# Kernel optimization log

Measured on AMD Instinct MI355X. Metric: run time of the kernel, lower is better.

Reference implementation:

```python
import jax, jax.numpy as jnp
import numpy as np

SCALE_XY = 1.2           # yolo1 in Yolov4Head
OBJ_THRESH = 0.5         # b_o >= 0.5 gate in post_process
BOX_SCORE_THRESH = 0.05
NMS_THRESH = 0.7         # rpn_nms_thresh
MAX_DET = 300            # fixed capacity for jit-compatible NMS


def _decode(x, anchors):
    # x: [B, A*(5+C), H, W] -> boxes [B,H,W,A,4] (xyxy, normalized), obj logits, class logits
    b, c, h, w = x.shape
    a = anchors.shape[0]
    nc = c // a - 5
    out = x.reshape(b, a, 5 + nc, h, w).transpose(0, 3, 4, 1, 2)  # [B,H,W,A,5+C]
    cx = jnp.arange(w, dtype=x.dtype).reshape(1, 1, w, 1)
    cy = jnp.arange(h, dtype=x.dtype).reshape(1, h, 1, 1)
    xy = SCALE_XY * jax.nn.sigmoid(out[..., :2]) - 0.5 * (SCALE_XY - 1)
    bx = (xy[..., 0] + cx) / w
    by = (xy[..., 1] + cy) / h
    b_xy = jnp.stack([bx, by], axis=-1)
    b_wh = jnp.clip(jnp.exp(out[..., 2:4]) * anchors.reshape(1, 1, 1, a, 2), 0.0, 2.0)
    tl = b_xy - 0.5 * b_wh
    boxes = jnp.concatenate([tl, tl + b_wh], axis=-1)  # [B,H,W,A,4]
    return boxes, out[..., 4], out[..., 5:]


def _iou_one_vs_all(box, boxes):
    lt = jnp.maximum(box[:2], boxes[:, :2])
    rb = jnp.minimum(box[2:], boxes[:, 2:])
    wh = jnp.clip(rb - lt, 0.0)
    inter = wh[:, 0] * wh[:, 1]
    a1 = (box[2] - box[0]) * (box[3] - box[1])
    a2 = (boxes[:, 2] - boxes[:, 0]) * (boxes[:, 3] - boxes[:, 1])
    return inter / (a1 + a2 - inter + 1e-9)


def _post_process_single(boxes, b_o, b_scores):
    # boxes [N,4], b_o [N], b_scores [N,C]; fixed-size equivalent of YoloLayer.post_process
    obj = jax.nn.sigmoid(b_o)
    cls = jax.nn.sigmoid(b_scores)
    boxes = jnp.clip(boxes, 0.0, 1.0)
    labels = jnp.argmax(cls, axis=-1)
    score = jnp.max(cls, axis=-1) * obj
    valid = (obj >= OBJ_THRESH) & (score >= BOX_SCORE_THRESH)
    masked = jnp.where(valid, score, -1.0)
    _, top_i = jax.lax.top_k(masked, MAX_DET)
    sel_boxes = boxes[top_i]
    sel_labels = labels[top_i]
    sel_valid = valid[top_i]
    sel_scores = jnp.where(sel_valid, score[top_i], 0.0)
    pos = jnp.arange(MAX_DET)

    def body(i, keep):
        iou = _iou_one_vs_all(sel_boxes[i], sel_boxes)
        suppress = (iou > NMS_THRESH) & keep[i] & (pos > i)
        return keep & (~suppress)

    keep = jax.lax.fori_loop(0, MAX_DET, body, sel_valid)
    return sel_boxes, sel_scores, sel_labels, keep


def setup_inputs() -> dict:
    key = jax.random.key(0)
    k1, _ = jax.random.split(key)
    x = jax.random.normal(k1, (32, 255, 76, 76), dtype=jnp.float32)
    anchors = jnp.array([[12.0, 16.0], [19.0, 36.0], [40.0, 28.0]], dtype=jnp.float32) / 608.0
    return {"x": x, "anchors": anchors}


def reference(x, anchors):
    boxes, b_o, b_s = _decode(x, anchors)
    b = x.shape[0]
    nc = b_s.shape[-1]
    boxes = boxes.reshape(b, -1, 4)
    b_o = b_o.reshape(b, -1)
    b_s = b_s.reshape(b, -1, nc)
    det_boxes, det_scores, det_labels, keep = jax.vmap(_post_process_single)(boxes, b_o, b_s)
    return det_boxes, det_scores, det_labels, keep
```

## Files before the change

### kernel.cpp

```cpp
#include <hip/hip_runtime.h>
#include <stdint.h>

#define BATCH   32
#define GRID_HW 5776
#define NA      3
#define NPB     (NA*GRID_HW)
#define NCLS    80
#define MAXDET  300
#define NBINS   4096
#define CANDN   512
#define T2      1024
#define CHUNK   17
#define NQ      (BATCH*NPB/4)
#define S4      (GRID_HW/4)

__device__ __forceinline__ float sigf(float x){ return 1.0f/(1.0f + expf(-x)); }

__device__ __forceinline__ int binf(float v){
    if (v < 0.0f) return 0;
    int b = (int)(v * 4096.0f);
    return b > (NBINS-1) ? (NBINS-1) : b;
}

__device__ __forceinline__ unsigned int ordf(float v){
    unsigned int u = __float_as_uint(v);
    return (u & 0x80000000u) ? ~u : (u | 0x80000000u);
}

__global__ void zero_hist_kernel(unsigned int* __restrict__ ghist)
{
    int i = blockIdx.x * blockDim.x + threadIdx.x;
    ghist[i] = 0u;
}

__global__ __launch_bounds__(256) void decode_kernel(const float* __restrict__ x,
                                                     const float* __restrict__ anchors,
                                                     float4* __restrict__ wbox,
                                                     float* __restrict__ wmsk,
                                                     int* __restrict__ wlab,
                                                     unsigned int* __restrict__ ghist)
{
    int tid = blockIdx.x * 256 + threadIdx.x;
    if (tid >= NQ) return;
    int b   = tid / (NPB/4);
    int r   = tid - b * (NPB/4);
    int a   = r / S4;
    int hw4 = r - a * S4;
    int hw0 = hw4 * 4;

    const float4* p4 = (const float4*)(x + (size_t)(b * 255 + a * 85) * GRID_HW) + hw4;

    float4 txv = p4[0];
    float4 tyv = p4[S4];
    float4 twv = p4[2*S4];
    float4 thv = p4[3*S4];
    float4 tov = p4[4*S4];

    float aw = anchors[a*2], ah = anchors[a*2+1];

    float bx0=-1.0f, bx1=-1.0f, bx2=-1.0f, bx3=-1.0f;
    int   l0=0, l1=0, l2=0, l3=0;
    const float4* pc = p4 + 5*S4;
    #pragma unroll 4
    for (int c = 0; c < NCLS; ++c){
        float4 v = pc[(size_t)c * S4];
        float s;
        s = sigf(v.x); if (s > bx0){ bx0 = s; l0 = c; }
        s = sigf(v.y); if (s > bx1){ bx1 = s; l1 = c; }
        s = sigf(v.z); if (s > bx2){ bx2 = s; l2 = c; }
        s = sigf(v.w); if (s > bx3){ bx3 = s; l3 = c; }
    }

    float tx[4] = {txv.x, txv.y, txv.z, txv.w};
    float ty[4] = {tyv.x, tyv.y, tyv.z, tyv.w};
    float tw[4] = {twv.x, twv.y, twv.z, twv.w};
    float th[4] = {thv.x, thv.y, thv.z, thv.w};
    float to[4] = {tov.x, tov.y, tov.z, tov.w};
    float bestv[4] = {bx0, bx1, bx2, bx3};
    int   bestl[4] = {l0, l1, l2, l3};

    #pragma unroll
    for (int j = 0; j < 4; ++j){
        int hw = hw0 + j;
        int h  = hw / 76;
        int w  = hw - h * 76;

        float sx = 1.2f * sigf(tx[j]) - 0.1f;
        float sy = 1.2f * sigf(ty[j]) - 0.1f;
        float bx = (sx + (float)w) / 76.0f;
        float by = (sy + (float)h) / 76.0f;
        float bw = fminf(fmaxf(expf(tw[j])*aw, 0.0f), 2.0f);
        float bh = fminf(fmaxf(expf(th[j])*ah, 0.0f), 2.0f);
        float tlx = bx - 0.5f*bw, tly = by - 0.5f*bh;
        float brx = tlx + bw,     bry = tly + bh;
        tlx = fminf(fmaxf(tlx,0.0f),1.0f);
        tly = fminf(fmaxf(tly,0.0f),1.0f);
        brx = fminf(fmaxf(brx,0.0f),1.0f);
        bry = fminf(fmaxf(bry,0.0f),1.0f);

        float obj = sigf(to[j]);
        float score = bestv[j] * obj;
        bool valid = (obj >= 0.5f) && (score >= 0.05f);

        int m = 4*tid + j;
        wbox[m] = make_float4(tlx, tly, brx, bry);
        wmsk[m] = valid ? score : -1.0f;
        wlab[m] = bestl[j];
        if (valid) atomicAdd(&ghist[b * NBINS + binf(score)], 1u);
    }
}

__global__ __launch_bounds__(T2) void postproc_kernel(const float4* __restrict__ wbox,
                                                      const float* __restrict__ wmsk,
                                                      const int* __restrict__ wlab,
                                                      const unsigned int* __restrict__ ghist,
                                                      float* __restrict__ out)
{
    __shared__ unsigned int shist[NBINS];
    __shared__ unsigned int wsum[16];
    __shared__ unsigned long long scan64[T2];
    __shared__ unsigned long long cand[CANDN];
    __shared__ float sbx[MAXDET], sby[MAXDET], sbz[MAXDET], sbw2[MAXDET];
    __shared__ float ssc[MAXDET];
    __shared__ int   slab[MAXDET];
    __shared__ unsigned long long adj[MAXDET][5];
    __shared__ unsigned long long kmask[5];
    __shared__ int s_bin, s_cnt;

    int t = threadIdx.x;
    int b = blockIdx.x;
    int wid = t >> 6, lane = t & 63;
    const float* msk = wmsk + (size_t)b * NPB;

    for (int i = t; i < NBINS; i += T2) shist[i] = ghist[b * NBINS + i];
    if (t == 0){ s_bin = -2; s_cnt = 0; }
    __syncthreads();

    unsigned int cs = shist[4*t] + shist[4*t+1] + shist[4*t+2] + shist[4*t+3];
    unsigned int vI = cs;
    #pragma unroll
    for (int d = 1; d < 64; d <<= 1){
        unsigned int o = __shfl_up(vI, d);
        if (lane >= d) vI += o;
    }
    if (lane == 63) wsum[wid] = vI;
    __syncthreads();
    if (t < 16){
        unsigned int s = wsum[t];
        #pragma unroll
        for (int d = 1; d < 16; d <<= 1){
            unsigned int o = __shfl_up(s, d);
            if (t >= d) s += o;
        }
        wsum[t] = s;
    }
    __syncthreads();
    unsigned int S = vI + (wid ? wsum[wid-1] : 0u);
    unsigned int total = wsum[15];
    if (total >= MAXDET){
        unsigned int c = total - S;
        #pragma unroll
        for (int k = 3; k >= 0; --k){
            unsigned int cg = c + shist[4*t + k];
            if (c < MAXDET && cg >= MAXDET) s_bin = 4*t + k;
            c = cg;
        }
    }
    __syncthreads();
    int cb = s_bin;

    if (cb >= 0){
        for (int m = t; m < NPB; m += T2){
            float v = msk[m];
            bool pred = (v >= 0.0f) && (binf(v) >= cb);
            unsigned long long bal = __ballot(pred);
            int cnt = __popcll(bal);
            if (cnt){
                int leader = __ffsll((long long)bal) - 1;
                int lbase = 0;
                if (lane == leader) lbase = atomicAdd(&s_cnt, cnt);
                int base = __shfl(lbase, leader);
                if (pred){
                    int off = __popcll(bal & ((1ull << lane) - 1ull));
                    int pos = base + off;
                    if (pos < CANDN){
                        int aidx = m / GRID_HW;
                        int hw   = m - aidx * GRID_HW;
                        unsigned int n = (unsigned int)(hw * 3 + aidx);
                        cand[pos] = ((unsigned long long)ordf(v) << 32) | (~n);
                    }
                }
            }
        }
    }
    __syncthreads();
    int cnum = s_cnt;
    bool exact = (cb >= 0) && (cnum <= CANDN);

    if (exact){
        for (int i = cnum + t; i < CANDN; i += T2) cand[i] = 0ull;
        __syncthreads();
        for (int k2 = 2; k2 <= CANDN; k2 <<= 1){
            for (int j = k2 >> 1; j > 0; j >>= 1){
                if (t < CANDN){
                    int ixj = t ^ j;
                    if (ixj > t){
                        unsigned long long a1 = cand[t], b1 = cand[ixj];
                        bool up = ((t & k2) == 0);
                        if ((a1 < b1) == up){ cand[t] = b1; cand[ixj] = a1; }
                    }
                }
                __syncthreads();
            }
        }
    } else {
        unsigned long long lk[CHUNK];
        int cstart = t * CHUNK;
        int ccnt = NPB - cstart; ccnt = ccnt < 0 ? 0 : (ccnt > CHUNK ? CHUNK : ccnt);
        for (int k = 0; k < CHUNK; ++k) lk[k] = 0ull;
        for (int k = 0; k < ccnt; ++k){
            int m = cstart + k;
            int aidx = m / GRID_HW;
            int hw   = m - aidx * GRID_HW;
            unsigned int n = (unsigned int)(hw * 3 + aidx);
            lk[k] = ((unsigned long long)ordf(msk[m]) << 32) | (~n);
        }
        for (int it = 0; it < MAXDET; ++it){
            unsigned long long lm = 0ull;
            for (int k = 0; k < CHUNK; ++k) lm = lk[k] > lm ? lk[k] : lm;
            scan64[t] = lm;
            __syncthreads();
            for (int s = T2 >> 1; s > 0; s >>= 1){
                if (t < s){ unsigned long long o = scan64[t+s]; if (o > scan64[t]) scan64[t] = o; }
                __syncthreads();
            }
            unsigned long long win = scan64[0];
            if (t == 0) cand[it] = win;
            for (int k = 0; k < CHUNK; ++k) if (lk[k] == win) lk[k] = 0ull;
            __syncthreads();
        }
        for (int i = MAXDET + t; i < CANDN; i += T2) cand[i] = 0ull;
        __syncthreads();
    }

    {
        bool valid = false;
        if (t < MAXDET){
            unsigned long long key = cand[t];
            unsigned int n = ~((unsigned int)key);
            int aidx = (int)(n % 3u);
            int hw   = (int)(n / 3u);
            int m    = aidx * GRID_HW + hw;
            float v  = msk[m];
            valid = v > -0.5f;
            float4 bb = wbox[(size_t)b * NPB + m];
            sbx[t] = bb.x; sby[t] = bb.y; sbz[t] = bb.z; sbw2[t] = bb.w;
            ssc[t] = valid ? v : 0.0f;
            slab[t] = wlab[(size_t)b * NPB + m];
        }
        if (wid < 5){
            unsigned long long bal = __ballot(valid);
            if (lane == 0) kmask[wid] = bal;
        }
    }
    __syncthreads();

    for (int task = wid; task < MAXDET*5; task += 16){
        int i  = task / 5;
        int w2 = task - i * 5;
        int j  = w2 * 64 + lane;
        int jc = j < MAXDET ? j : (MAXDET-1);
        float lx = fmaxf(sbx[i], sbx[jc]);
        float ly = fmaxf(sby[i], sby[jc]);
        float rx = fminf(sbz[i], sbz[jc]);
        float ry = fminf(sbw2[i], sbw2[jc]);
        float iw = fmaxf(rx - lx, 0.0f);
        float ih = fmaxf(ry - ly, 0.0f);
        float inter = iw * ih;
        float a1 = (sbz[i]-sbx[i]) * (sbw2[i]-sby[i]);
        float a2 = (sbz[jc]-sbx[jc]) * (sbw2[jc]-sby[jc]);
        float iou = inter / (a1 + a2 - inter + 1e-9f);
        bool pred = (j < MAXDET) && (j > i) && (iou > 0.7f);
        unsigned long long bal = __ballot(pred);
        if (lane == 0) adj[i][w2] = bal;
    }
    __syncthreads();

    if (t < 64){
        unsigned long long km0 = kmask[0], km1 = kmask[1], km2 = kmask[2],
                           km3 = kmask[3], km4 = kmask[4];
        #define NMS_BLK(B, LIM, KM)                                            \
        for (int i2 = 0; i2 < (LIM); ++i2){                                    \
            int i = (B)*64 + i2;                                               \
            unsigned long long m2 = ((KM >> i2) & 1ull) ? ~0ull : 0ull;        \
            km0 &= ~(adj[i][0] & m2);                                          \
            km1 &= ~(adj[i][1] & m2);                                          \
            km2 &= ~(adj[i][2] & m2);                                          \
            km3 &= ~(adj[i][3] & m2);                                          \
            km4 &= ~(adj[i][4] & m2);                                          \
        }
        NMS_BLK(0, 64, km0)
        NMS_BLK(1, 64, km1)
        NMS_BLK(2, 64, km2)
        NMS_BLK(3, 64, km3)
        NMS_BLK(4, 44, km4)
        #undef NMS_BLK
        if (t == 0){
            kmask[0] = km0; kmask[1] = km1; kmask[2] = km2;
            kmask[3] = km3; kmask[4] = km4;
        }
    }
    __syncthreads();

    if (t < MAXDET){
        float* ob = out + (size_t)b * (MAXDET*4) + (size_t)t * 4;
        ob[0] = sbx[t]; ob[1] = sby[t]; ob[2] = sbz[t]; ob[3] = sbw2[t];
        out[BATCH*MAXDET*4 + b*MAXDET + t] = ssc[t];
        out[BATCH*MAXDET*5 + b*MAXDET + t] = (float)slab[t];
        out[BATCH*MAXDET*6 + b*MAXDET + t] = ((kmask[t >> 6] >> (t & 63)) & 1ull) ? 1.0f : 0.0f;
    }
}

extern "C" void kernel_launch(void* const* d_in, const int* in_sizes, int n_in,
                              void* d_out, int out_size, void* d_ws, size_t ws_size,
                              hipStream_t stream)
{
    const float* x       = (const float*)d_in[0];
    const float* anchors = (const float*)d_in[1];
    float* out = (float*)d_out;

    char* ws = (char*)d_ws;
    float4*       wbox  = (float4*)ws;
    float*        wmsk  = (float*)(ws + (size_t)BATCH*NPB*16);
    int*          wlab  = (int*)  (ws + (size_t)BATCH*NPB*20);
    unsigned int* ghist = (unsigned int*)(ws + (size_t)BATCH*NPB*24);

    zero_hist_kernel<<<(BATCH*NBINS)/256, 256, 0, stream>>>(ghist);
    decode_kernel<<<(NQ + 255)/256, 256, 0, stream>>>(x, anchors, wbox, wmsk, wlab, ghist);
    postproc_kernel<<<BATCH, T2, 0, stream>>>(wbox, wmsk, wlab, ghist, out);
}
```

Baseline: 357.0 us.

## Decode boxes only for selected candidates and build histogram in shared memory

The decode kernel no longer computes or writes boxes for every anchor, and no longer builds the global score histogram with atomics. The histogram is now built per batch inside the postproc kernel from the mask array using shared-memory atomics. Box decoding is done only for the top candidates, reading raw x directly. This removes the large box write, the four extra input loads, the global atomics and the zero kernel. In exchange the postproc kernel, which runs only 32 blocks, must rescan the full mask per batch.

```diff
diff --git a/kernel.cpp b/kernel.cpp
--- a/kernel.cpp
+++ b/kernel.cpp
@@ -27,18 +27,9 @@
     return (u & 0x80000000u) ? ~u : (u | 0x80000000u);
 }
 
-__global__ void zero_hist_kernel(unsigned int* __restrict__ ghist)
-{
-    int i = blockIdx.x * blockDim.x + threadIdx.x;
-    ghist[i] = 0u;
-}
-
 __global__ __launch_bounds__(256) void decode_kernel(const float* __restrict__ x,
-                                                     const float* __restrict__ anchors,
-                                                     float4* __restrict__ wbox,
                                                      float* __restrict__ wmsk,
-                                                     int* __restrict__ wlab,
-                                                     unsigned int* __restrict__ ghist)
+                                                     int* __restrict__ wlab)
 {
     int tid = blockIdx.x * 256 + threadIdx.x;
     if (tid >= NQ) return;
@@ -46,17 +37,10 @@
     int r   = tid - b * (NPB/4);
     int a   = r / S4;
     int hw4 = r - a * S4;
-    int hw0 = hw4 * 4;
 
     const float4* p4 = (const float4*)(x + (size_t)(b * 255 + a * 85) * GRID_HW) + hw4;
 
-    float4 txv = p4[0];
-    float4 tyv = p4[S4];
-    float4 twv = p4[2*S4];
-    float4 thv = p4[3*S4];
     float4 tov = p4[4*S4];
-
-    float aw = anchors[a*2], ah = anchors[a*2+1];
 
     float bx0=-1.0f, bx1=-1.0f, bx2=-1.0f, bx3=-1.0f;
     int   l0=0, l1=0, l2=0, l3=0;
@@ -71,49 +55,26 @@
         s = sigf(v.w); if (s > bx3){ bx3 = s; l3 = c; }
     }
 
-    float tx[4] = {txv.x, txv.y, txv.z, txv.w};
-    float ty[4] = {tyv.x, tyv.y, tyv.z, tyv.w};
-    float tw[4] = {twv.x, twv.y, twv.z, twv.w};
-    float th[4] = {thv.x, thv.y, thv.z, thv.w};
-    float to[4] = {tov.x, tov.y, tov.z, tov.w};
+    float to[4]    = {tov.x, tov.y, tov.z, tov.w};
     float bestv[4] = {bx0, bx1, bx2, bx3};
     int   bestl[4] = {l0, l1, l2, l3};
 
     #pragma unroll
     for (int j = 0; j < 4; ++j){
-        int hw = hw0 + j;
-        int h  = hw / 76;
-        int w  = hw - h * 76;
-
-        float sx = 1.2f * sigf(tx[j]) - 0.1f;
-        float sy = 1.2f * sigf(ty[j]) - 0.1f;
-        float bx = (sx + (float)w) / 76.0f;
-        float by = (sy + (float)h) / 76.0f;
-        float bw = fminf(fmaxf(expf(tw[j])*aw, 0.0f), 2.0f);
-        float bh = fminf(fmaxf(expf(th[j])*ah, 0.0f), 2.0f);
-        float tlx = bx - 0.5f*bw, tly = by - 0.5f*bh;
-        float brx = tlx + bw,     bry = tly + bh;
-        tlx = fminf(fmaxf(tlx,0.0f),1.0f);
-        tly = fminf(fmaxf(tly,0.0f),1.0f);
-        brx = fminf(fmaxf(brx,0.0f),1.0f);
-        bry = fminf(fmaxf(bry,0.0f),1.0f);
-
         float obj = sigf(to[j]);
         float score = bestv[j] * obj;
         bool valid = (obj >= 0.5f) && (score >= 0.05f);
 
         int m = 4*tid + j;
-        wbox[m] = make_float4(tlx, tly, brx, bry);
         wmsk[m] = valid ? score : -1.0f;
         wlab[m] = bestl[j];
-        if (valid) atomicAdd(&ghist[b * NBINS + binf(score)], 1u);
-    }
-}
-
-__global__ __launch_bounds__(T2) void postproc_kernel(const float4* __restrict__ wbox,
+    }
+}
+
+__global__ __launch_bounds__(T2) void postproc_kernel(const float* __restrict__ x,
+                                                      const float* __restrict__ anchors,
                                                       const float* __restrict__ wmsk,
                                                       const int* __restrict__ wlab,
-                                                      const unsigned int* __restrict__ ghist,
                                                       float* __restrict__ out)
 {
     __shared__ unsigned int shist[NBINS];
@@ -132,8 +93,13 @@
     int wid = t >> 6, lane = t & 63;
     const float* msk = wmsk + (size_t)b * NPB;
 
-    for (int i = t; i < NBINS; i += T2) shist[i] = ghist[b * NBINS + i];
+    for (int i = t; i < NBINS; i += T2) shist[i] = 0u;
     if (t == 0){ s_bin = -2; s_cnt = 0; }
+    __syncthreads();
+    for (int m = t; m < NPB; m += T2){
+        float v = msk[m];
+        if (v >= 0.0f) atomicAdd(&shist[binf(v)], 1u);
+    }
     __syncthreads();
 
     unsigned int cs = shist[4*t] + shist[4*t+1] + shist[4*t+2] + shist[4*t+3];
@@ -253,9 +219,30 @@
             int m    = aidx * GRID_HW + hw;
             float v  = msk[m];
             valid = v > -0.5f;
-            float4 bb = wbox[(size_t)b * NPB + m];
-            sbx[t] = bb.x; sby[t] = bb.y; sbz[t] = bb.z; sbw2[t] = bb.w;
-            ssc[t] = valid ? v : 0.0f;
+
+            int h = hw / 76;
+            int w = hw - h * 76;
+            const float* p = x + (size_t)(b * 255 + aidx * 85) * GRID_HW + hw;
+            float tx = p[0];
+            float ty = p[GRID_HW];
+            float tw = p[2*GRID_HW];
+            float th = p[3*GRID_HW];
+            float aw = anchors[aidx*2], ah = anchors[aidx*2+1];
+
+            float sx = 1.2f * sigf(tx) - 0.1f;
+            float sy = 1.2f * sigf(ty) - 0.1f;
+            float bxc = (sx + (float)w) / 76.0f;
+            float byc = (sy + (float)h) / 76.0f;
+            float bw = fminf(fmaxf(expf(tw)*aw, 0.0f), 2.0f);
+            float bh = fminf(fmaxf(expf(th)*ah, 0.0f), 2.0f);
+            float tlx = bxc - 0.5f*bw, tly = byc - 0.5f*bh;
+            float brx = tlx + bw,      bry = tly + bh;
+
+            sbx[t]  = fminf(fmaxf(tlx,0.0f),1.0f);
+            sby[t]  = fminf(fmaxf(tly,0.0f),1.0f);
+            sbz[t]  = fminf(fmaxf(brx,0.0f),1.0f);
+            sbw2[t] = fminf(fmaxf(bry,0.0f),1.0f);
+            ssc[t]  = valid ? v : 0.0f;
             slab[t] = wlab[(size_t)b * NPB + m];
         }
         if (wid < 5){
@@ -330,12 +317,9 @@
     float* out = (float*)d_out;
 
     char* ws = (char*)d_ws;
-    float4*       wbox  = (float4*)ws;
-    float*        wmsk  = (float*)(ws + (size_t)BATCH*NPB*16);
-    int*          wlab  = (int*)  (ws + (size_t)BATCH*NPB*20);
-    unsigned int* ghist = (unsigned int*)(ws + (size_t)BATCH*NPB*24);
-
-    zero_hist_kernel<<<(BATCH*NBINS)/256, 256, 0, stream>>>(ghist);
-    decode_kernel<<<(NQ + 255)/256, 256, 0, stream>>>(x, anchors, wbox, wmsk, wlab, ghist);
-    postproc_kernel<<<BATCH, T2, 0, stream>>>(wbox, wmsk, wlab, ghist, out);
-}
+    float* wmsk = (float*)ws;
+    int*   wlab = (int*)(ws + (size_t)BATCH*NPB*4);
+
+    decode_kernel<<<(NQ + 255)/256, 256, 0, stream>>>(x, wmsk, wlab);
+    postproc_kernel<<<BATCH, T2, 0, stream>>>(x, anchors, wmsk, wlab, out);
+}
```

Result: faster. 349.5 us (-2.1%).
